# Performance work log

Hardware: AMD Instinct MI355X
Metric: run time of the kernel (lower is better)

Reference implementation:

```python
import jax, jax.numpy as jnp
import numpy as np
from jax import lax

N = 100_000      # active voxels
C = 64           # nIn == nOut
K = 343          # 7*7*7 depthwise taps
HID = 4 * C      # pointwise expansion
EPS = 1e-5
CENTER = K // 2  # self offset


def setup_inputs() -> dict:
    key = jax.random.key(0)
    ks = jax.random.split(key, 10)
    x_feat = jax.random.normal(ks[0], (N, C), dtype=jnp.float32)
    nbr = jax.random.randint(ks[1], (N, K), 0, N, dtype=jnp.int32)
    valid = jax.random.uniform(ks[2], (N, K)) < 0.25
    nbr = jnp.where(valid, nbr, jnp.int32(N))
    nbr = nbr.at[:, CENTER].set(jnp.arange(N, dtype=jnp.int32))  # submanifold: center is self
    W1 = jax.random.normal(ks[3], (K, C), dtype=jnp.float32) * 0.05
    b1 = jax.random.normal(ks[4], (C,), dtype=jnp.float32) * 0.02
    gamma = jnp.ones((C,), dtype=jnp.float32)
    beta = jnp.zeros((C,), dtype=jnp.float32)
    W2 = jax.random.normal(ks[5], (C, HID), dtype=jnp.float32) * (1.0 / np.sqrt(C))
    b2 = jax.random.normal(ks[6], (HID,), dtype=jnp.float32) * 0.02
    W3 = jax.random.normal(ks[7], (HID, C), dtype=jnp.float32) * (1.0 / np.sqrt(HID))
    b3 = jax.random.normal(ks[8], (C,), dtype=jnp.float32) * 0.02
    return {"x_feat": x_feat, "nbr_idx": nbr, "W1": W1, "b1": b1,
            "gamma": gamma, "beta": beta, "W2": W2, "b2": b2, "W3": W3, "b3": b3}


def _depthwise_submanifold(feat, nbr_idx, W1, b1):
    # feat [N,C]; nbr_idx [N,K] with sentinel N -> zero contribution
    feat_pad = jnp.concatenate([feat, jnp.zeros((1, feat.shape[1]), feat.dtype)], axis=0)
    def step(acc, xs):
        idx_k, w_k = xs                       # [N], [C]
        return acc + feat_pad[idx_k] * w_k, None  # gather + per-channel MAC
    acc0 = jnp.zeros_like(feat)
    out, _ = lax.scan(step, acc0, (nbr_idx.T, W1))  # scan over K=343 taps
    return out + b1


def _groupnorm1(h, gamma, beta):
    # num_groups=1 over channels, per active site
    mu = jnp.mean(h, axis=-1, keepdims=True)
    var = jnp.var(h, axis=-1, keepdims=True)
    return (h - mu) * lax.rsqrt(var + EPS) * gamma + beta


def reference(x_feat, nbr_idx, W1, b1, gamma, beta, W2, b2, W3, b3):
    h = _depthwise_submanifold(x_feat, nbr_idx, W1, b1)  # conv1 (depthwise 7^3)
    h = _groupnorm1(h, gamma, beta)                      # norm
    h = h @ W2 + b2                                      # conv2 (1x1x1, C->4C)
    h = jax.nn.gelu(h, approximate=False)                # exact GELU (torch default)
    h = h @ W3 + b3                                      # conv3 (1x1x1, 4C->C)
    return h + x_feat                                    # residual add
```

## Files before the change

kernel.cpp:

```cpp
#include <hip/hip_runtime.h>
#include <hip/hip_fp16.h>
#include <math.h>

#define CH    64
#define KT    343
#define HIDD  256
#define KCAP  144

typedef __attribute__((ext_vector_type(8))) _Float16 half8;
typedef __attribute__((ext_vector_type(4))) _Float16 half4;
typedef __attribute__((ext_vector_type(4))) float f32x4;
struct H24 { __half2 x, y, z, w; };

#define MEMBAR() asm volatile("" ::: "memory")

#define PRELOAD6(v, w)                                                     \
  { const int* row_ = nbr + (size_t)(w) * KT;                              \
    _Pragma("unroll") for (int p = 0; p < 6; ++p) {                        \
      const int tap_ = p * 64 + lane;                                      \
      v[p] = (tap_ < KT) ? row_[tap_] : N; } }

__global__ __launch_bounds__(256) void prep_compact_kernel(
    const float* __restrict__ W1, const float* __restrict__ W2,
    const float* __restrict__ W3, const float* __restrict__ x,
    const int* __restrict__ nbr, _Float16* __restrict__ W1h,
    _Float16* __restrict__ W2Th, _Float16* __restrict__ W3Th,
    _Float16* __restrict__ xh, int* __restrict__ packed,
    int* __restrict__ cnt, int N, int nelem) {
  const int t = blockIdx.x * 256 + threadIdx.x;
  const int step = gridDim.x * 256;
  for (int e = t; e < KT * CH; e += step) W1h[e] = (_Float16)W1[e];
  for (int e = t; e < CH * HIDD; e += step) {
    int k = e >> 8, n = e & 255;
    W2Th[n * CH + k] = (_Float16)W2[e];
  }
  for (int e = t; e < HIDD * CH; e += step) {
    int k = e >> 6, n = e & 63;
    W3Th[n * HIDD + k] = (_Float16)W3[e];
  }
  const int tot4 = nelem / 4 + 16;
  for (int q = t; q < tot4; q += step) {
    const int eb = q * 4;
    float4 v = (eb < nelem) ? *(const float4*)(x + eb) : make_float4(0.f, 0.f, 0.f, 0.f);
    half4 o;
    o[0] = (_Float16)v.x; o[1] = (_Float16)v.y;
    o[2] = (_Float16)v.z; o[3] = (_Float16)v.w;
    *(half4*)(xh + eb) = o;
  }

  const int lane = threadIdx.x & 63;
  const int wv = t >> 6;
  const int nw = (gridDim.x * 256) >> 6;
  int w = wv;
  if (w < N) {
    int v[6];
    PRELOAD6(v, w);
    while (w < N) {
      const int wn = w + nw;
      int vn[6];
      if (wn < N) PRELOAD6(vn, wn);
      int* prow = packed + (size_t)w * KCAP;
      int base = 0;
#pragma unroll
      for (int p = 0; p < 6; ++p) {
        const int tap = p * 64 + lane;
        const bool valid = (tap < KT) && (v[p] != N);
        const unsigned long long m = __ballot(valid);
        const int pos = __popcll(m & ((1ull << lane) - 1ull));
        if (valid) {
          const int wp = base + pos;
          if (wp < KCAP) prow[wp] = v[p] | (tap << 17);
        }
        base += __popcll(m);
      }
      if (lane == 0) cnt[w] = (base < KCAP) ? base : KCAP;
      w = wn;
#pragma unroll
      for (int p = 0; p < 6; ++p) v[p] = vn[p];
    }
  }
}

#define ISSUE8(buf, vi)                                                     \
  { _Pragma("unroll") for (int p = 0; p < 8; ++p) {                         \
      const int pk_ = __builtin_amdgcn_ds_bpermute(pb + 4 * p, (vi));       \
      buf[p] = *(const uint4*)(xb + ((((unsigned)pk_ & 0x1FFFFu) << 7) + (unsigned)e16)); } }

#define CONSUME8(buf, vi)                                                   \
  { _Pragma("unroll") for (int p = 0; p < 8; ++p) {                         \
      const int pk_ = __builtin_amdgcn_ds_bpermute(pb + 4 * p, (vi));       \
      const uint4 wq_ = *(const uint4*)(w1b + ((((unsigned)pk_) >> 17) << 7) + (unsigned)e16); \
      const H24 gh_ = __builtin_bit_cast(H24, buf[p]);                      \
      const H24 wh_ = __builtin_bit_cast(H24, wq_);                         \
      acc0 = __hfma2(gh_.x, wh_.x, acc0);                                   \
      acc1 = __hfma2(gh_.y, wh_.y, acc1);                                   \
      acc2 = __hfma2(gh_.z, wh_.z, acc2);                                   \
      acc3 = __hfma2(gh_.w, wh_.w, acc3); } }

__global__ __launch_bounds__(256, 3) void fused_kernel(
    const _Float16* __restrict__ xh, const float* __restrict__ x,
    const int* __restrict__ packed, const int* __restrict__ cnt,
    const _Float16* __restrict__ W1h,
    const float* __restrict__ b1, const float* __restrict__ gamma,
    const float* __restrict__ beta, const _Float16* __restrict__ W2Th,
    const float* __restrict__ b2, const _Float16* __restrict__ W3Th,
    const float* __restrict__ b3, float* __restrict__ out, int N) {
  __shared__ __align__(16) _Float16 hs[32][CH + 8];
  __shared__ __align__(16) _Float16 gs[32][HIDD + 8];

  const int t = threadIdx.x;
  const int wvid = t >> 6;
  const int lane = t & 63;
  const int g = lane >> 3;
  const int e = lane & 7;
  const int e16 = e << 4;
  const int pb = (lane & 56) << 2;
  const int vbase = blockIdx.x * 32;
  const int vb = __builtin_amdgcn_readfirstlane(vbase + wvid * 8);

  const int cnt_g = cnt[vb + g];
  int mx = cnt_g;
  mx = max(mx, __shfl_xor(mx, 8));
  mx = max(mx, __shfl_xor(mx, 16));
  mx = max(mx, __shfl_xor(mx, 32));
  const int nck2 = __builtin_amdgcn_readfirstlane((((mx + 7) >> 3) + 1) & ~1);
  const int* prow = packed + (size_t)(vb + g) * KCAP;
  const int PADV = N;
  const char* xb = (const char*)xh;
  const char* w1b = (const char*)W1h;

  __half2 acc0 = __float2half2_rn(0.f), acc1 = acc0, acc2 = acc0, acc3 = acc0;

  uint4 ga[8], gb[8];

  #define LDE(ck) ( (((ck) * 8 + e) < cnt_g) ? prow[(ck) * 8 + e] : PADV )

  int viA = LDE(0);
  int viB = LDE(1);
  ISSUE8(ga, viA);

  for (int ck = 0; ck < nck2; ck += 2) {
    const int viC = (ck + 2 < nck2) ? LDE(ck + 2) : PADV;
    MEMBAR();
    ISSUE8(gb, viB);
    MEMBAR();
    CONSUME8(ga, viA);
    const int viD = (ck + 3 < nck2) ? LDE(ck + 3) : PADV;
    MEMBAR();
    if (ck + 2 < nck2) ISSUE8(ga, viC);
    MEMBAR();
    CONSUME8(gb, viB);
    viA = viC;
    viB = viD;
  }

  float fa[8];
  fa[0] = __low2float(acc0); fa[1] = __high2float(acc0);
  fa[2] = __low2float(acc1); fa[3] = __high2float(acc1);
  fa[4] = __low2float(acc2); fa[5] = __high2float(acc2);
  fa[6] = __low2float(acc3); fa[7] = __high2float(acc3);
  {
    float4 blo = *(const float4*)(b1 + e * 8);
    float4 bhi = *(const float4*)(b1 + e * 8 + 4);
    fa[0] += blo.x; fa[1] += blo.y; fa[2] += blo.z; fa[3] += blo.w;
    fa[4] += bhi.x; fa[5] += bhi.y; fa[6] += bhi.z; fa[7] += bhi.w;
  }
  float s = 0.f, ss = 0.f;
#pragma unroll
  for (int d = 0; d < 8; ++d) { s += fa[d]; ss += fa[d] * fa[d]; }
  s += __shfl_xor(s, 1); ss += __shfl_xor(ss, 1);
  s += __shfl_xor(s, 2); ss += __shfl_xor(ss, 2);
  s += __shfl_xor(s, 4); ss += __shfl_xor(ss, 4);
  const float mu = s * (1.0f / 64.0f);
  const float var = ss * (1.0f / 64.0f) - mu * mu;
  const float inv = rsqrtf(var + 1e-5f);
  {
    float4 glo = *(const float4*)(gamma + e * 8);
    float4 ghi = *(const float4*)(gamma + e * 8 + 4);
    float4 tlo = *(const float4*)(beta + e * 8);
    float4 thi = *(const float4*)(beta + e * 8 + 4);
    const float gm[8] = {glo.x, glo.y, glo.z, glo.w, ghi.x, ghi.y, ghi.z, ghi.w};
    const float bt[8] = {tlo.x, tlo.y, tlo.z, tlo.w, thi.x, thi.y, thi.z, thi.w};
    half8 hv;
#pragma unroll
    for (int d = 0; d < 8; ++d)
      hv[d] = (_Float16)((fa[d] - mu) * inv * gm[d] + bt[d]);
    *(half8*)&hs[wvid * 8 + g][e * 8] = hv;
  }
  __syncthreads();

  const int row16 = lane & 15, quad = lane >> 4;
  half8 afr[2][2];
#pragma unroll
  for (int rt = 0; rt < 2; ++rt)
#pragma unroll
    for (int ks = 0; ks < 2; ++ks)
      afr[rt][ks] = *(const half8*)&hs[rt * 16 + row16][ks * 32 + quad * 8];

#pragma unroll
  for (int cl = 0; cl < 4; ++cl) {
    const int n = wvid * 64 + cl * 16 + row16;
    f32x4 a0 = {0.f, 0.f, 0.f, 0.f}, a1 = {0.f, 0.f, 0.f, 0.f};
#pragma unroll
    for (int ks = 0; ks < 2; ++ks) {
      half8 bfr = *(const half8*)(W2Th + (size_t)n * CH + ks * 32 + quad * 8);
      a0 = __builtin_amdgcn_mfma_f32_16x16x32_f16(afr[0][ks], bfr, a0, 0, 0, 0);
      a1 = __builtin_amdgcn_mfma_f32_16x16x32_f16(afr[1][ks], bfr, a1, 0, 0, 0);
    }
    const float bias = b2[n];
#pragma unroll
    for (int r = 0; r < 4; ++r) {
      float z0 = a0[r] + bias;
      float z1 = a1[r] + bias;
      gs[quad * 4 + r][n]      = (_Float16)(0.5f * z0 * (1.0f + erff(z0 * 0.70710678118654752f)));
      gs[16 + quad * 4 + r][n] = (_Float16)(0.5f * z1 * (1.0f + erff(z1 * 0.70710678118654752f)));
    }
  }
  __syncthreads();

  f32x4 o0 = {0.f, 0.f, 0.f, 0.f}, o1 = {0.f, 0.f, 0.f, 0.f};
  const int oc = wvid * 16 + row16;
#pragma unroll
  for (int ks = 0; ks < 8; ++ks) {
    half8 bfr = *(const half8*)(W3Th + (size_t)oc * HIDD + ks * 32 + quad * 8);
    half8 a20 = *(const half8*)&gs[row16][ks * 32 + quad * 8];
    half8 a21 = *(const half8*)&gs[16 + row16][ks * 32 + quad * 8];
    o0 = __builtin_amdgcn_mfma_f32_16x16x32_f16(a20, bfr, o0, 0, 0, 0);
    o1 = __builtin_amdgcn_mfma_f32_16x16x32_f16(a21, bfr, o1, 0, 0, 0);
  }
  const float bias3 = b3[oc];
#pragma unroll
  for (int r = 0; r < 4; ++r) {
    size_t v0 = (size_t)vbase + quad * 4 + r;
    size_t v1 = (size_t)vbase + 16 + quad * 4 + r;
    out[v0 * CH + oc] = o0[r] + bias3 + x[v0 * CH + oc];
    out[v1 * CH + oc] = o1[r] + bias3 + x[v1 * CH + oc];
  }
}

extern "C" void kernel_launch(void* const* d_in, const int* in_sizes, int n_in,
                              void* d_out, int out_size, void* d_ws, size_t ws_size,
                              hipStream_t stream) {
  const float* x_feat = (const float*)d_in[0];
  const int*   nbr    = (const int*)d_in[1];
  const float* W1     = (const float*)d_in[2];
  const float* b1     = (const float*)d_in[3];
  const float* gamma  = (const float*)d_in[4];
  const float* beta   = (const float*)d_in[5];
  const float* W2     = (const float*)d_in[6];
  const float* b2     = (const float*)d_in[7];
  const float* W3     = (const float*)d_in[8];
  const float* b3     = (const float*)d_in[9];
  float* out = (float*)d_out;

  const int N = in_sizes[0] / CH;

  char* ws = (char*)d_ws;
  size_t off = 0;
  _Float16* xh = (_Float16*)(ws + off);
  off += (((size_t)(N + 1) * CH * 2) + 255) & ~(size_t)255;
  _Float16* W1h = (_Float16*)(ws + off);
  off += ((size_t)KT * CH * 2 + 255) & ~(size_t)255;
  _Float16* W2Th = (_Float16*)(ws + off);
  off += ((size_t)HIDD * CH * 2 + 255) & ~(size_t)255;
  _Float16* W3Th = (_Float16*)(ws + off);
  off += ((size_t)CH * HIDD * 2 + 255) & ~(size_t)255;
  int* packed = (int*)(ws + off);
  off += ((size_t)N * KCAP * 4 + 255) & ~(size_t)255;
  int* cnt = (int*)(ws + off);
  off += ((size_t)N * 4 + 255) & ~(size_t)255;

  hipLaunchKernelGGL(prep_compact_kernel, dim3(2048), dim3(256), 0, stream,
                     W1, W2, W3, x_feat, nbr, W1h, W2Th, W3Th, xh,
                     packed, cnt, N, N * CH);
  hipLaunchKernelGGL(fused_kernel, dim3(N / 32), dim3(256), 0, stream,
                     xh, x_feat, packed, cnt, W1h, b1, gamma, beta,
                     W2Th, b2, W3Th, b3, out, N);
}
```

Before: 445.7 us.

## Split fused kernel into conv and MLP kernels, stage W1 in LDS

Splits the fused depthwise-conv+norm+MLP kernel into two kernels: a conv kernel with 512-thread blocks that stages the whole fp16 W1 table (about 43 KB) in LDS and writes the normalized fp16 activations to a global buffer, and a separate MLP kernel that reads them back for the MFMA pointwise layers. The goal is to serve the per-tap weight loads from LDS instead of global/L1 and to let each phase pick its own occupancy and LDS budget. In exchange it adds an extra global round-trip of N×64 halfs, a third kernel launch, and a per-block copy of W1 into LDS. The prep kernel grid is also doubled.

```diff
diff --git a/kernel.cpp b/kernel.cpp
--- a/kernel.cpp
+++ b/kernel.cpp
@@ -89,7 +89,7 @@
 #define CONSUME8(buf, vi)                                                   \
   { _Pragma("unroll") for (int p = 0; p < 8; ++p) {                         \
       const int pk_ = __builtin_amdgcn_ds_bpermute(pb + 4 * p, (vi));       \
-      const uint4 wq_ = *(const uint4*)(w1b + ((((unsigned)pk_) >> 17) << 7) + (unsigned)e16); \
+      const uint4 wq_ = *(const uint4*)&W1s[((((unsigned)pk_) >> 17) << 7) + e16]; \
       const H24 gh_ = __builtin_bit_cast(H24, buf[p]);                      \
       const H24 wh_ = __builtin_bit_cast(H24, wq_);                         \
       acc0 = __hfma2(gh_.x, wh_.x, acc0);                                   \
@@ -97,16 +97,12 @@
       acc2 = __hfma2(gh_.z, wh_.z, acc2);                                   \
       acc3 = __hfma2(gh_.w, wh_.w, acc3); } }
 
-__global__ __launch_bounds__(256, 3) void fused_kernel(
-    const _Float16* __restrict__ xh, const float* __restrict__ x,
-    const int* __restrict__ packed, const int* __restrict__ cnt,
-    const _Float16* __restrict__ W1h,
+__global__ __launch_bounds__(512, 2) void conv_kernel(
+    const _Float16* __restrict__ xh, const int* __restrict__ packed,
+    const int* __restrict__ cnt, const _Float16* __restrict__ W1h,
     const float* __restrict__ b1, const float* __restrict__ gamma,
-    const float* __restrict__ beta, const _Float16* __restrict__ W2Th,
-    const float* __restrict__ b2, const _Float16* __restrict__ W3Th,
-    const float* __restrict__ b3, float* __restrict__ out, int N) {
-  __shared__ __align__(16) _Float16 hs[32][CH + 8];
-  __shared__ __align__(16) _Float16 gs[32][HIDD + 8];
+    const float* __restrict__ beta, _Float16* __restrict__ h, int N) {
+  __shared__ __align__(16) char W1s[43904];
 
   const int t = threadIdx.x;
   const int wvid = t >> 6;
@@ -115,8 +111,14 @@
   const int e = lane & 7;
   const int e16 = e << 4;
   const int pb = (lane & 56) << 2;
-  const int vbase = blockIdx.x * 32;
-  const int vb = __builtin_amdgcn_readfirstlane(vbase + wvid * 8);
+  const int vbase = blockIdx.x * 64;
+  const int vb = __builtin_amdgcn_readfirstlane(min(vbase + wvid * 8, N - 8));
+
+  {
+    const uint4* src = (const uint4*)W1h;
+    uint4* dst = (uint4*)W1s;
+    for (int q = t; q < 2744; q += 512) dst[q] = src[q];
+  }
 
   const int cnt_g = cnt[vb + g];
   int mx = cnt_g;
@@ -127,7 +129,6 @@
   const int* prow = packed + (size_t)(vb + g) * KCAP;
   const int PADV = N;
   const char* xb = (const char*)xh;
-  const char* w1b = (const char*)W1h;
 
   __half2 acc0 = __float2half2_rn(0.f), acc1 = acc0, acc2 = acc0, acc3 = acc0;
 
@@ -138,6 +139,7 @@
   int viA = LDE(0);
   int viB = LDE(1);
   ISSUE8(ga, viA);
+  __syncthreads();
 
   for (int ck = 0; ck < nck2; ck += 2) {
     const int viC = (ck + 2 < nck2) ? LDE(ck + 2) : PADV;
@@ -185,17 +187,29 @@
 #pragma unroll
     for (int d = 0; d < 8; ++d)
       hv[d] = (_Float16)((fa[d] - mu) * inv * gm[d] + bt[d]);
-    *(half8*)&hs[wvid * 8 + g][e * 8] = hv;
-  }
-  __syncthreads();
-
+    *(half8*)&h[(size_t)(vb + g) * CH + e * 8] = hv;
+  }
+}
+
+__global__ __launch_bounds__(256, 2) void mlp_kernel(
+    const _Float16* __restrict__ h, const float* __restrict__ x,
+    const _Float16* __restrict__ W2Th, const float* __restrict__ b2,
+    const _Float16* __restrict__ W3Th, const float* __restrict__ b3,
+    float* __restrict__ out, int N) {
+  __shared__ __align__(16) _Float16 gs[32][HIDD + 8];
+
+  const int t = threadIdx.x;
+  const int wvid = t >> 6;
+  const int lane = t & 63;
+  const int vbase = blockIdx.x * 32;
   const int row16 = lane & 15, quad = lane >> 4;
+
   half8 afr[2][2];
 #pragma unroll
   for (int rt = 0; rt < 2; ++rt)
 #pragma unroll
     for (int ks = 0; ks < 2; ++ks)
-      afr[rt][ks] = *(const half8*)&hs[rt * 16 + row16][ks * 32 + quad * 8];
+      afr[rt][ks] = *(const half8*)(h + (size_t)(vbase + rt * 16 + row16) * CH + ks * 32 + quad * 8);
 
 #pragma unroll
   for (int cl = 0; cl < 4; ++cl) {
@@ -269,11 +283,14 @@
   off += ((size_t)N * KCAP * 4 + 255) & ~(size_t)255;
   int* cnt = (int*)(ws + off);
   off += ((size_t)N * 4 + 255) & ~(size_t)255;
-
-  hipLaunchKernelGGL(prep_compact_kernel, dim3(2048), dim3(256), 0, stream,
+  _Float16* h = (_Float16*)(ws + off);
+  off += ((size_t)N * CH * 2 + 255) & ~(size_t)255;
+
+  hipLaunchKernelGGL(prep_compact_kernel, dim3(4096), dim3(256), 0, stream,
                      W1, W2, W3, x_feat, nbr, W1h, W2Th, W3Th, xh,
                      packed, cnt, N, N * CH);
-  hipLaunchKernelGGL(fused_kernel, dim3(N / 32), dim3(256), 0, stream,
-                     xh, x_feat, packed, cnt, W1h, b1, gamma, beta,
-                     W2Th, b2, W3Th, b3, out, N);
-}
+  hipLaunchKernelGGL(conv_kernel, dim3((N + 63) / 64), dim3(512), 0, stream,
+                     xh, packed, cnt, W1h, b1, gamma, beta, h, N);
+  hipLaunchKernelGGL(mlp_kernel, dim3(N / 32), dim3(256), 0, stream,
+                     h, x_feat, W2Th, b2, W3Th, b3, out, N);
+}
```

Result: faster. 422.8 us (-5.1%).
